# Kernel tuning notes

Hardware: AMD Instinct MI355X
Metric: run time of the kernel (lower is better)

## Reference

```python
import jax, jax.numpy as jnp
import numpy as np


def _pairwise_sqdist(x, y):
    # x: [B,N,D], y: [B,M,D] -> P: [B,N,M] squared euclidean distances
    xx = jnp.sum(x * x, axis=-1)            # [B,N]
    yy = jnp.sum(y * y, axis=-1)            # [B,M]
    zz = jnp.einsum('bnd,bmd->bnm', x, y)   # [B,N,M]
    return xx[:, :, None] + yy[:, None, :] - 2.0 * zz


def setup_inputs() -> dict:
    key = jax.random.key(0)
    k1, k2 = jax.random.split(key)
    B, N, M, D = 8, 4096, 4096, 256
    gts = jax.random.normal(k1, (B, N, D), dtype=jnp.float32)
    preds = jax.random.normal(k2, (B, M, D), dtype=jnp.float32)
    return {"gts": gts, "preds": preds}


def reference(gts, preds):
    P = _pairwise_sqdist(gts, preds)        # [B,N,M]
    loss_1 = jnp.sum(jnp.min(P, axis=1))    # min over gts dim (axis=1)
    loss_2 = jnp.sum(jnp.min(P, axis=2))    # min over preds dim (axis=2)
    return loss_1 + loss_2
```

## Files before the change

### kernel.cpp

```cpp
#include <hip/hip_runtime.h>

typedef int   i32x8 __attribute__((ext_vector_type(8)));
typedef float f32x4 __attribute__((ext_vector_type(4)));

#define B_   8
#define N_   4096
#define D_   256


__device__ __forceinline__ void gl_lds16(const void* g, void* l) {
  __builtin_amdgcn_global_load_lds(
      (const __attribute__((address_space(1))) unsigned int*)g,
      (__attribute__((address_space(3))) unsigned int*)l, 16, 0, 0);
}

__device__ __forceinline__ float sq8(unsigned w) {
  float f0 = __builtin_amdgcn_cvt_f32_fp8(w, 0);
  float f1 = __builtin_amdgcn_cvt_f32_fp8(w, 1);
  float f2 = __builtin_amdgcn_cvt_f32_fp8(w, 2);
  float f3 = __builtin_amdgcn_cvt_f32_fp8(w, 3);
  return f0 * f0 + f1 * f1 + f2 * f2 + f3 * f3;
}

__global__ __launch_bounds__(256) void prep_kernel(
    const float* __restrict__ x, const float* __restrict__ y,
    unsigned char* __restrict__ Xf, unsigned char* __restrict__ Yf,
    float* __restrict__ xx, float* __restrict__ yy,
    unsigned* __restrict__ rowmin, unsigned* __restrict__ colmin,
    float* __restrict__ out)
{
  __shared__ unsigned char T[4][16 * 272];
  if (blockIdx.x == 0 && threadIdx.x == 0) out[0] = 0.f;

  const int wv = threadIdx.x >> 6, lane = threadIdx.x & 63;
  const int wid = (blockIdx.x << 2) + wv;

  const float* src; unsigned char* dst; float* nrm; unsigned* mn; int g;
  if (wid < 2048) { g = wid;        src = x; dst = Xf; nrm = xx; mn = rowmin; }
  else            { g = wid - 2048; src = y; dst = Yf; nrm = yy; mn = colmin; }

  unsigned char* tw = T[wv];
  const float* rp = src + (size_t)g * 16 * D_;
#pragma unroll
  for (int r = 0; r < 16; ++r) {
    float4 v = *(const float4*)(rp + r * D_ + lane * 4);
    unsigned u = __builtin_amdgcn_cvt_pk_fp8_f32(v.x, v.y, 0, 0);
    u = __builtin_amdgcn_cvt_pk_fp8_f32(v.z, v.w, u, 1);
    *(unsigned*)(tw + r * 272 + lane * 4) = u;
  }
  asm volatile("s_waitcnt lgkmcnt(0)" ::: "memory");
  __builtin_amdgcn_wave_barrier();

  float s = 0.f;
  const int row = lane & 15, ko = (lane >> 4) * 32;
#pragma unroll
  for (int kt = 0; kt < 2; ++kt)
#pragma unroll
    for (int h = 0; h < 2; ++h) {
      uint4 c = *(const uint4*)(tw + row * 272 + kt * 128 + ko + h * 16);
      s += sq8(c.x) + sq8(c.y) + sq8(c.z) + sq8(c.w);
      *(uint4*)(dst + ((((size_t)g * 2 + kt) * 2 + h) << 10) + lane * 16) = c;
    }
  s += __shfl_xor(s, 16, 64);
  s += __shfl_xor(s, 32, 64);
  if      (lane < 16) nrm[g * 16 + lane] = s;
  else if (lane < 32) mn[g * 16 + lane - 16] = 0x7f800000u;
}

__global__ __launch_bounds__(256, 2) void chamfer_gemm(
    const unsigned char* __restrict__ Xf, const unsigned char* __restrict__ Yf,
    const float* __restrict__ xx, const float* __restrict__ yy,
    unsigned* __restrict__ rowmin, unsigned* __restrict__ colmin)
{
  __shared__ __align__(16) unsigned char S[4][8192];
  __shared__ unsigned cmin_s[512];
  __shared__ float    yys[512];

  const int bid = blockIdx.x;
  const int b   = bid & 7;
  const int rt  = (bid >> 3) & 15;
  const int cq  = bid >> 7;
  const int n0  = rt * 256;
  const int m0  = cq * 512;

  const int t = threadIdx.x, lane = t & 63, wave = t >> 6;
  const int quad = lane >> 4, lcol = lane & 15;

  cmin_s[t]       = 0x7f800000u;
  cmin_s[t + 256] = 0x7f800000u;
  const float* yyp = yy + b * N_ + m0;
  if (t < 128)
    gl_lds16((const unsigned char*)yyp + t * 16, (unsigned char*)yys + t * 16);

  i32x8 af[4][2];
#pragma unroll
  for (int i = 0; i < 4; ++i) {
    const size_t g = (size_t)(b * 256 + rt * 16 + wave * 4 + i);
#pragma unroll
    for (int kt = 0; kt < 2; ++kt) {
      const uint4* p = (const uint4*)(Xf + ((g * 2 + kt) << 11));
      uint4* h = (uint4*)&af[i][kt];
      h[0] = p[lane];
      h[1] = p[64 + lane];
    }
  }

  float xv[4][4], rmin[4][4];
  const float* xxp = xx + b * N_ + n0 + wave * 64;
#pragma unroll
  for (int i = 0; i < 4; ++i)
#pragma unroll
    for (int r = 0; r < 4; ++r) {
      xv[i][r] = xxp[i * 16 + quad * 4 + r];
      rmin[i][r] = 1e30f;
    }

  const unsigned char* Ybase = Yf + ((size_t)(b * 256 + cq * 32) << 12);

#define STAGE_B(ct_, buf_)                                                    \
  {                                                                           \
    const unsigned char* Ysrc = Ybase + ((size_t)(ct_) << 13);     \
    _Pragma("unroll")                                                         \
    for (int h2 = 0; h2 < 2; ++h2) {                                          \
      int s  = t + h2 * 256;                                                  \
      int cd = s >> 6, ln = s & 63;                                           \
      int kt = cd >> 2, hh = (cd >> 1) & 1, jj = cd & 1;                      \
      gl_lds16(Ysrc + jj * 4096 + kt * 2048 + hh * 1024 + ln * 16,            \
               (buf_) + s * 16);                                              \
    }                                                                         \
  }

  STAGE_B(0, S[0]);
  STAGE_B(1, S[1]);
  STAGE_B(2, S[2]);
  __syncthreads();

  auto do_ct = [&](int ct, const unsigned char* curb) {
    i32x8 bq[2][2];
#pragma unroll
    for (int j = 0; j < 2; ++j)
#pragma unroll
      for (int kt = 0; kt < 2; ++kt) {
        uint4* h = (uint4*)&bq[j][kt];
        h[0] = *(const uint4*)(curb + (kt * 4 + 0 + j) * 1024 + lane * 16);
        h[1] = *(const uint4*)(curb + (kt * 4 + 2 + j) * 1024 + lane * 16);
      }

    f32x4 acc[4][2] = {};
    __builtin_amdgcn_s_setprio(1);
#pragma unroll
    for (int kt = 0; kt < 2; ++kt)
#pragma unroll
      for (int i = 0; i < 4; ++i)
#pragma unroll
        for (int j = 0; j < 2; ++j)
          acc[i][j] = __builtin_amdgcn_mfma_scale_f32_16x16x128_f8f6f4(
              af[i][kt], bq[j][kt], acc[i][j],
              0, 0,
              0, 127,
              0, 127);
    __builtin_amdgcn_s_setprio(0);

#pragma unroll
    for (int j = 0; j < 2; ++j) {
      float yv = yys[ct * 32 + j * 16 + lcol];
      float tc[16];
#pragma unroll
      for (int i = 0; i < 4; ++i)
#pragma unroll
        for (int r = 0; r < 4; ++r) {
          float a = acc[i][j][r];
          rmin[i][r] = fminf(rmin[i][r], __builtin_fmaf(-2.0f, a, yv));
          tc[i * 4 + r] = __builtin_fmaf(-2.0f, a, xv[i][r]);
        }
      float m0_ = fminf(fminf(tc[0], tc[1]), fminf(tc[2], tc[3]));
      float m1_ = fminf(fminf(tc[4], tc[5]), fminf(tc[6], tc[7]));
      float m2_ = fminf(fminf(tc[8], tc[9]), fminf(tc[10], tc[11]));
      float m3_ = fminf(fminf(tc[12], tc[13]), fminf(tc[14], tc[15]));
      float cm  = fminf(fminf(m0_, m1_), fminf(m2_, m3_));
      atomicMin(&cmin_s[ct * 32 + j * 16 + lcol], __float_as_uint(cm + yv));
    }
  };

  for (int ct = 0; ct < 14; ++ct) {
    asm volatile("s_waitcnt vmcnt(4)" ::: "memory");
    __builtin_amdgcn_s_barrier();
    if (ct < 13) STAGE_B(ct + 3, S[(ct + 3) & 3]);
    do_ct(ct, S[ct & 3]);
  }
  asm volatile("s_waitcnt vmcnt(2)" ::: "memory");
  __builtin_amdgcn_s_barrier();
  do_ct(14, S[14 & 3]);
  asm volatile("s_waitcnt vmcnt(0)" ::: "memory");
  __builtin_amdgcn_s_barrier();
  do_ct(15, S[15 & 3]);

#pragma unroll
  for (int i = 0; i < 4; ++i)
#pragma unroll
    for (int r = 0; r < 4; ++r) {
      float v = xv[i][r] + rmin[i][r];
#pragma unroll
      for (int m = 1; m < 16; m <<= 1) v = fminf(v, __shfl_xor(v, m, 64));
      if (lcol == 0)
        atomicMin(rowmin + b * N_ + n0 + wave * 64 + i * 16 + quad * 4 + r,
                  __float_as_uint(v));
    }

  __syncthreads();
#pragma unroll
  for (int i = 0; i < 2; ++i) {
    int idx = t + i * 256;
    atomicMin(colmin + b * N_ + m0 + idx, cmin_s[idx]);
  }
#undef STAGE_B
}

__global__ __launch_bounds__(256) void reduce_kernel(
    const unsigned* __restrict__ mins,
    float* __restrict__ out)
{
  int idx = blockIdx.x * 256 + threadIdx.x;
  uint4 u = ((const uint4*)mins)[idx];
  float s = __uint_as_float(u.x) + __uint_as_float(u.y)
          + __uint_as_float(u.z) + __uint_as_float(u.w);
#pragma unroll
  for (int m = 1; m < 64; m <<= 1) s += __shfl_xor(s, m, 64);
  if ((threadIdx.x & 63) == 0) atomicAdd(out, s);
}

extern "C" void kernel_launch(void* const* d_in, const int* in_sizes, int n_in,
                              void* d_out, int out_size, void* d_ws, size_t ws_size,
                              hipStream_t stream) {
  const float* gts   = (const float*)d_in[0];
  const float* preds = (const float*)d_in[1];

  char* ws = (char*)d_ws;
  const size_t XB_BYTES = (size_t)B_ * N_ * D_;
  unsigned char* Xf     = (unsigned char*)ws;
  unsigned char* Yf     = (unsigned char*)(ws + XB_BYTES);
  float*    xx     = (float*)(ws + 2 * XB_BYTES);
  float*    yy     = (float*)(ws + 2 * XB_BYTES + (size_t)B_ * N_ * 4);
  unsigned* rowmin = (unsigned*)(ws + 2 * XB_BYTES + (size_t)B_ * N_ * 8);
  unsigned* colmin = (unsigned*)(ws + 2 * XB_BYTES + (size_t)B_ * N_ * 12);

  prep_kernel<<<1024, 256, 0, stream>>>(gts, preds, Xf, Yf, xx, yy, rowmin, colmin,
                                        (float*)d_out);

  chamfer_gemm<<<1024, 256, 0, stream>>>(Xf, Yf, xx, yy, rowmin, colmin);

  reduce_kernel<<<64, 256, 0, stream>>>(rowmin, (float*)d_out);
}
```

Baseline: 137.7 us.

## Load B tiles directly from global memory instead of LDS multi-buffer pipeline

Removes the 4-deep LDS staging ring for the Y operand, along with its async global-to-LDS loads, waitcnt and per-tile barriers. Each wave now reads its B fragments straight from global memory, relying on L1/L2 because all waves in the block share the same tile. It also starts the first MFMA of each k-step from a zero accumulator instead of zero-initializing. This frees LDS and removes block-wide synchronization, but exposes global load latency with no explicit prefetch and reads the same data four times per block.

Result: no change. 137.9 us (+0.1%).

```diff
diff --git a/kernel.cpp b/kernel.cpp
--- a/kernel.cpp
+++ b/kernel.cpp
@@ -72,7 +72,6 @@
     const float* __restrict__ xx, const float* __restrict__ yy,
     unsigned* __restrict__ rowmin, unsigned* __restrict__ colmin)
 {
-  __shared__ __align__(16) unsigned char S[4][8192];
   __shared__ unsigned cmin_s[512];
   __shared__ float    yys[512];
 
@@ -115,50 +114,40 @@
       rmin[i][r] = 1e30f;
     }
 
+  __syncthreads();
+
   const unsigned char* Ybase = Yf + ((size_t)(b * 256 + cq * 32) << 12);
-
-#define STAGE_B(ct_, buf_)                                                    \
-  {                                                                           \
-    const unsigned char* Ysrc = Ybase + ((size_t)(ct_) << 13);     \
-    _Pragma("unroll")                                                         \
-    for (int h2 = 0; h2 < 2; ++h2) {                                          \
-      int s  = t + h2 * 256;                                                  \
-      int cd = s >> 6, ln = s & 63;                                           \
-      int kt = cd >> 2, hh = (cd >> 1) & 1, jj = cd & 1;                      \
-      gl_lds16(Ysrc + jj * 4096 + kt * 2048 + hh * 1024 + ln * 16,            \
-               (buf_) + s * 16);                                              \
-    }                                                                         \
-  }
-
-  STAGE_B(0, S[0]);
-  STAGE_B(1, S[1]);
-  STAGE_B(2, S[2]);
-  __syncthreads();
-
-  auto do_ct = [&](int ct, const unsigned char* curb) {
+  const f32x4 z4 = {0.f, 0.f, 0.f, 0.f};
+
+  for (int ct = 0; ct < 16; ++ct) {
+    const unsigned char* Yct = Ybase + ((size_t)ct << 13);
+
     i32x8 bq[2][2];
 #pragma unroll
     for (int j = 0; j < 2; ++j)
 #pragma unroll
       for (int kt = 0; kt < 2; ++kt) {
         uint4* h = (uint4*)&bq[j][kt];
-        h[0] = *(const uint4*)(curb + (kt * 4 + 0 + j) * 1024 + lane * 16);
-        h[1] = *(const uint4*)(curb + (kt * 4 + 2 + j) * 1024 + lane * 16);
+        h[0] = *(const uint4*)(Yct + j * 4096 + kt * 2048 + lane * 16);
+        h[1] = *(const uint4*)(Yct + j * 4096 + kt * 2048 + 1024 + lane * 16);
       }
 
-    f32x4 acc[4][2] = {};
+    f32x4 acc[4][2];
     __builtin_amdgcn_s_setprio(1);
 #pragma unroll
-    for (int kt = 0; kt < 2; ++kt)
-#pragma unroll
-      for (int i = 0; i < 4; ++i)
-#pragma unroll
-        for (int j = 0; j < 2; ++j)
-          acc[i][j] = __builtin_amdgcn_mfma_scale_f32_16x16x128_f8f6f4(
-              af[i][kt], bq[j][kt], acc[i][j],
-              0, 0,
-              0, 127,
-              0, 127);
+    for (int i = 0; i < 4; ++i)
+#pragma unroll
+      for (int j = 0; j < 2; ++j)
+        acc[i][j] = __builtin_amdgcn_mfma_scale_f32_16x16x128_f8f6f4(
+            af[i][0], bq[j][0], z4,
+            0, 0, 0, 127, 0, 127);
+#pragma unroll
+    for (int i = 0; i < 4; ++i)
+#pragma unroll
+      for (int j = 0; j < 2; ++j)
+        acc[i][j] = __builtin_amdgcn_mfma_scale_f32_16x16x128_f8f6f4(
+            af[i][1], bq[j][1], acc[i][j],
+            0, 0, 0, 127, 0, 127);
     __builtin_amdgcn_s_setprio(0);
 
 #pragma unroll
@@ -180,20 +169,7 @@
       float cm  = fminf(fminf(m0_, m1_), fminf(m2_, m3_));
       atomicMin(&cmin_s[ct * 32 + j * 16 + lcol], __float_as_uint(cm + yv));
     }
-  };
-
-  for (int ct = 0; ct < 14; ++ct) {
-    asm volatile("s_waitcnt vmcnt(4)" ::: "memory");
-    __builtin_amdgcn_s_barrier();
-    if (ct < 13) STAGE_B(ct + 3, S[(ct + 3) & 3]);
-    do_ct(ct, S[ct & 3]);
-  }
-  asm volatile("s_waitcnt vmcnt(2)" ::: "memory");
-  __builtin_amdgcn_s_barrier();
-  do_ct(14, S[14 & 3]);
-  asm volatile("s_waitcnt vmcnt(0)" ::: "memory");
-  __builtin_amdgcn_s_barrier();
-  do_ct(15, S[15 & 3]);
+  }
 
 #pragma unroll
   for (int i = 0; i < 4; ++i)
@@ -213,7 +189,6 @@
     int idx = t + i * 256;
     atomicMin(colmin + b * N_ + m0 + idx, cmin_s[idx]);
   }
-#undef STAGE_B
 }
 
 __global__ __launch_bounds__(256) void reduce_kernel(
```
